# Optimization experiments

Hardware: AMD Instinct MI355X
Metric: run time of the kernel (lower is better)

## Reference

```python
import jax, jax.numpy as jnp
import numpy as np

SEQ_LEN = 8192
D_MODEL = 1024
D_K = 128
D_V = 128


def setup_inputs() -> dict:
    key = jax.random.key(0)
    kx, kq, kk, kv = jax.random.split(key, 4)
    # xavier-uniform scale for (out, in) linear weights
    def xavier(k, out_f, in_f):
        lim = np.sqrt(6.0 / (in_f + out_f))
        return jax.random.uniform(k, (out_f, in_f), jnp.float32, -lim, lim)
    return {
        "X": jax.random.normal(kx, (SEQ_LEN, D_MODEL), jnp.float32),
        "Wq": xavier(kq, D_K, D_MODEL),
        "Wk": xavier(kk, D_K, D_MODEL),
        "Wv": xavier(kv, D_V, D_MODEL),
    }


def reference(X, Wq, Wk, Wv):
    # X: (S, d_model); W*: (d_k, d_model) torch Linear weights (y = x @ W.T)
    S = X.shape[0]
    Q = X @ Wq.T                      # (S, d_k)
    K = X @ Wk.T                      # (S, d_k)
    V = X @ Wv.T                      # (S, d_v)
    scale = jnp.sqrt(jnp.asarray(D_K, X.dtype))
    scores = (Q @ K.T) / scale        # (S, S)
    causal = jnp.tril(jnp.ones((S, S), bool))
    scores = jnp.where(causal, scores, -jnp.inf)
    weights = jax.nn.softmax(scores, axis=1)
    # dropout p=0.0 -> identity
    Z = weights @ V                   # (S, d_v)
    return Z
```

## Files before the change

kernel.cpp:

```cpp
#include <hip/hip_runtime.h>
#include <hip/hip_bf16.h>

#define S_LEN 8192
#define DM    1024
#define DK    128
#define KSTR  136
#define VSTR  72
#define PSTR2 72
#define SLOTD 1056

typedef __attribute__((ext_vector_type(8))) short bf16x8;
typedef __attribute__((ext_vector_type(8))) _Float16 f16x8;
typedef __attribute__((ext_vector_type(4))) float f32x4;

__device__ __forceinline__ f32x4 mfma16(bf16x8 a, bf16x8 b, f32x4 c) {
    return __builtin_amdgcn_mfma_f32_16x16x32_bf16(a, b, c, 0, 0, 0);
}

__device__ __forceinline__ ushort f2bf(float f) {
    unsigned u = __builtin_bit_cast(unsigned, f);
    u += 0x7FFFu + ((u >> 16) & 1u);
    return (ushort)(u >> 16);
}

__device__ __forceinline__ ushort f2h(float f) {
    return __builtin_bit_cast(ushort, (_Float16)f);
}

__global__ __launch_bounds__(256, 1)
void convert_kernel(const float* __restrict__ X,
                    const float* __restrict__ Wq,
                    const float* __restrict__ Wk,
                    const float* __restrict__ Wv,
                    _Float16* __restrict__ Xh,
                    _Float16* __restrict__ Wh) {
    const int NX4 = S_LEN * DM / 4;
    const int NW4 = DK * DM / 4;
    const int total4 = NX4 + 3 * NW4;
    for (int i = blockIdx.x * 256 + threadIdx.x; i < total4; i += gridDim.x * 256) {
        const float4* src;
        _Float16* dst;
        int off;
        if (i < NX4) {
            src = (const float4*)X; dst = Xh; off = i;
        } else {
            const int w = i - NX4;
            const int which = w / NW4;
            off = w - which * NW4;
            src = (const float4*)(which == 0 ? Wq : (which == 1 ? Wk : Wv));
            dst = Wh + which * (DK * DM);
        }
        const float4 v = src[off];
        union { _Float16 h[4]; uint2 u; } p;
        p.h[0] = (_Float16)v.x; p.h[1] = (_Float16)v.y;
        p.h[2] = (_Float16)v.z; p.h[3] = (_Float16)v.w;
        *(uint2*)(dst + (size_t)off * 4) = p.u;
    }
}

__global__ __launch_bounds__(256)
void proj_gemm_kernel(const _Float16* __restrict__ Xh,
                      const _Float16* __restrict__ Wh,
                      ushort* __restrict__ Qb,
                      ushort* __restrict__ Kb,
                      ushort* __restrict__ Vtb) {
    __shared__ _Float16 Ash[32 * 32];
    __shared__ _Float16 Bsh[128 * 32];

    const int tid  = threadIdx.x;
    const int lane = tid & 63;
    const int quad = lane >> 4;
    const int l15  = lane & 15;
    const int wv   = tid >> 6;
    const int wm   = wv & 1;
    const int wn   = wv >> 1;
    const int m0   = blockIdx.x * 32;
    const int nb   = blockIdx.y;
    const _Float16* Wbase = Wh + nb * (DK * DM);

    f32x4 acc[4];
#pragma unroll
    for (int ni = 0; ni < 4; ++ni) acc[ni] = (f32x4){0.f, 0.f, 0.f, 0.f};

    for (int kk = 0; kk < DM; kk += 32) {
        __syncthreads();
        for (int s = tid; s < 640; s += 256) {
            if (s < 128) {
                const int row = s >> 2, sg = s & 3;
                __builtin_amdgcn_global_load_lds(
                    (const __attribute__((address_space(1))) void*)(Xh + (size_t)(m0 + row) * DM + kk + sg * 8),
                    (__attribute__((address_space(3))) void*)(Ash + s * 8), 16, 0, 0);
            } else {
                const int t = s - 128;
                const int row = t >> 2, sg = t & 3;
                __builtin_amdgcn_global_load_lds(
                    (const __attribute__((address_space(1))) void*)(Wbase + (size_t)row * DM + kk + sg * 8),
                    (__attribute__((address_space(3))) void*)(Bsh + t * 8), 16, 0, 0);
            }
        }
        __syncthreads();

        const f16x8 af = *(const f16x8*)(Ash + (wm * 16 + l15) * 32 + quad * 8);
        f16x8 bf[4];
#pragma unroll
        for (int t = 0; t < 4; ++t)
            bf[t] = *(const f16x8*)(Bsh + (wn * 64 + t * 16 + l15) * 32 + quad * 8);
#pragma unroll
        for (int ni = 0; ni < 4; ++ni)
            acc[ni] = __builtin_amdgcn_mfma_f32_16x16x32_f16(af, bf[ni], acc[ni], 0, 0, 0);
    }

    if (nb == 2) {
#pragma unroll
        for (int ni = 0; ni < 4; ++ni) {
            const int n = wn * 64 + ni * 16 + l15;
            const int m = m0 + wm * 16 + quad * 4;
            union { ushort h[4]; uint2 u; } p;
#pragma unroll
            for (int r = 0; r < 4; ++r) p.h[r] = f2bf(acc[ni][r]);
            *(uint2*)(Vtb + (size_t)n * S_LEN + m) = p.u;
        }
    } else {
        ushort* Ob = (nb == 0) ? Qb : Kb;
        const float sc = (nb == 0) ? 0.088388347648318447f * 1.4426950408889634f : 1.0f;
#pragma unroll
        for (int ni = 0; ni < 4; ++ni) {
            const int n = wn * 64 + ni * 16 + l15;
#pragma unroll
            for (int r = 0; r < 4; ++r) {
                const int m = m0 + wm * 16 + quad * 4 + r;
                Ob[(size_t)m * DK + n] = f2bf(acc[ni][r] * sc);
            }
        }
    }
}

__global__ __launch_bounds__(256, 3)
void flash_partial_kernel(const ushort* __restrict__ Qg,
                          const ushort* __restrict__ Kg,
                          const ushort* __restrict__ Vtg,
                          float* __restrict__ Part) {
    __shared__ __align__(16) ushort Ks [64 * KSTR];
    __shared__ __align__(16) ushort Vts[128 * VSTR];
    __shared__ __align__(16) ushort PlA[4 * 16 * PSTR2];

    const int b = 575 - (int)blockIdx.x;
    int g = 0;
    while (b >= 8 * (g + 1) * (g + 2)) ++g;
    const int idx   = b - 8 * g * (g + 1);
    const int qb    = 16 * g + idx / (g + 1);
    const int chunk = idx % (g + 1);
    const int nkt   = qb + 1;
    const int kt_lo = chunk * nkt / (g + 1);
    const int kt_hi = (chunk + 1) * nkt / (g + 1);

    const int tid  = threadIdx.x;
    const int wv   = tid >> 6;
    const int lane = tid & 63;
    const int quad = lane >> 4;
    const int l15  = lane & 15;
    const int q0w  = qb * 64 + wv * 16;
    ushort* Pl = PlA + wv * 16 * PSTR2;

    bf16x8 qf[4];
    {
        const ushort* qrow = Qg + (size_t)(q0w + l15) * DK + quad * 8;
#pragma unroll
        for (int kc = 0; kc < 4; ++kc) qf[kc] = *(const bf16x8*)(qrow + kc * 32);
    }

    const bf16x8 ones = {(short)0x3F80, (short)0x3F80, (short)0x3F80, (short)0x3F80,
                         (short)0x3F80, (short)0x3F80, (short)0x3F80, (short)0x3F80};

    float m_[4], l_[4];
#pragma unroll
    for (int r = 0; r < 4; ++r) { m_[r] = -__builtin_inff(); l_[r] = 0.f; }
    f32x4 acc[8];
#pragma unroll
    for (int d = 0; d < 8; ++d) acc[d] = (f32x4){0.f, 0.f, 0.f, 0.f};

    bf16x8 stg[8];
#define LOAD_TILE(K0)                                                          \
    {                                                                          \
        const int k0_ = (K0);                                                  \
        _Pragma("unroll")                                                      \
        for (int i = 0; i < 8; ++i) {                                          \
            const int c = tid + (i << 8);                                      \
            if (c < 1024) {                                                    \
                const int row = c >> 4, ch = c & 15;                           \
                stg[i] = *(const bf16x8*)(Kg + (size_t)(k0_ + row) * DK + ch * 8); \
            } else {                                                           \
                const int cc = c - 1024;                                       \
                const int row = cc >> 3, ch = cc & 7;                          \
                stg[i] = *(const bf16x8*)(Vtg + (size_t)row * S_LEN + k0_ + ch * 8); \
            }                                                                  \
        }                                                                      \
    }

    LOAD_TILE(kt_lo * 64)

    for (int kt = kt_lo; kt < kt_hi; ++kt) {
        const int k0 = kt * 64;

        __syncthreads();
#pragma unroll
        for (int i = 0; i < 8; ++i) {
            const int c = tid + (i << 8);
            if (c < 1024) {
                const int row = c >> 4, ch = c & 15;
                *(bf16x8*)(Ks + row * KSTR + ch * 8) = stg[i];
            } else {
                const int cc = c - 1024;
                const int row = cc >> 3, ch = cc & 7;
                *(bf16x8*)(Vts + row * VSTR + ch * 8) = stg[i];
            }
        }
        if (kt + 1 < kt_hi) LOAD_TILE((kt + 1) * 64)
        __syncthreads();

        f32x4 Sr[4];
#pragma unroll
        for (int nb = 0; nb < 4; ++nb) {
            Sr[nb] = (f32x4){0.f, 0.f, 0.f, 0.f};
            const ushort* kb = Ks + (nb * 16 + l15) * KSTR + quad * 8;
#pragma unroll
            for (int kc = 0; kc < 4; ++kc)
                Sr[nb] = mfma16(qf[kc], *(const bf16x8*)(kb + kc * 32), Sr[nb]);
        }

        if (k0 + 63 > q0w) {
#pragma unroll
            for (int nb = 0; nb < 4; ++nb) {
                const int kg = k0 + nb * 16 + l15;
#pragma unroll
                for (int r = 0; r < 4; ++r)
                    if (kg > q0w + quad * 4 + r) Sr[nb][r] = -__builtin_inff();
            }
        }

        float al[4];
#pragma unroll
        for (int r = 0; r < 4; ++r) {
            float v = m_[r];
#pragma unroll
            for (int nb = 0; nb < 4; ++nb) v = fmaxf(v, Sr[nb][r]);
            v = fmaxf(v, __shfl_xor(v, 1));
            v = fmaxf(v, __shfl_xor(v, 2));
            v = fmaxf(v, __shfl_xor(v, 4));
            v = fmaxf(v, __shfl_xor(v, 8));
            al[r] = exp2f(m_[r] - v);
            m_[r] = v;
        }
#pragma unroll
        for (int nb = 0; nb < 4; ++nb) {
#pragma unroll
            for (int r = 0; r < 4; ++r) {
                const float p = exp2f(Sr[nb][r] - m_[r]);
                Pl[(quad * 4 + r) * PSTR2 + nb * 16 + l15] = f2bf(p);
            }
        }
#pragma unroll
        for (int d = 0; d < 8; ++d)
#pragma unroll
            for (int r = 0; r < 4; ++r) acc[d][r] *= al[r];

        f32x4 sacc = (f32x4){0.f, 0.f, 0.f, 0.f};
#pragma unroll
        for (int kcp = 0; kcp < 2; ++kcp) {
            const bf16x8 pf = *(const bf16x8*)(Pl + l15 * PSTR2 + kcp * 32 + quad * 8);
            sacc = mfma16(pf, ones, sacc);
#pragma unroll
            for (int db = 0; db < 8; ++db) {
                const bf16x8 vf = *(const bf16x8*)(Vts + (db * 16 + l15) * VSTR + kcp * 32 + quad * 8);
                acc[db] = mfma16(pf, vf, acc[db]);
            }
        }
#pragma unroll
        for (int r = 0; r < 4; ++r) l_[r] = l_[r] * al[r] + sacc[r];
    }
#undef LOAD_TILE

    const int qt16 = qb * 4 + wv;
    float* slot = Part + (size_t)(qt16 * 8 + chunk) * SLOTD;
    if (l15 == 0) {
#pragma unroll
        for (int r = 0; r < 4; ++r) {
            slot[quad * 4 + r]      = m_[r];
            slot[16 + quad * 4 + r] = l_[r];
        }
    }
    uint* slotO = (uint*)(slot + 32);
#pragma unroll
    for (int d = 0; d < 8; ++d)
#pragma unroll
        for (int r = 0; r < 4; ++r) {
            const float v  = acc[d][r];
            const float vp = __shfl_xor(v, 1);
            if ((l15 & 1) == 0) {
                const int row = quad * 4 + r;
                const uint u = (uint)f2h(v) | ((uint)f2h(vp) << 16);
                slotO[(row * 128 + d * 16 + l15) >> 1] = u;
            }
        }
}

__global__ __launch_bounds__(256)
void flash_merge_kernel(const float* __restrict__ Part, float* __restrict__ Out) {
    __shared__ float Ms[16], Ls[16];
    __shared__ float Sc[8][16];
    const int qt = blockIdx.x;
    const int q0 = qt * 16;
    const int P  = (qt >> 6) + 1;
    const int tid = threadIdx.x;
    const float* base = Part + (size_t)qt * 8 * SLOTD;

    if (tid < 16) {
        float M = -__builtin_inff();
        for (int p = 0; p < P; ++p) M = fmaxf(M, base[p * SLOTD + tid]);
        float L = 0.f;
        for (int p = 0; p < P; ++p)
            L += base[p * SLOTD + 16 + tid] * exp2f(base[p * SLOTD + tid] - M);
        Ms[tid] = M; Ls[tid] = L;
    }
    __syncthreads();
    if (tid < 128) {
        const int p = tid >> 4, row = tid & 15;
        Sc[p][row] = (p < P) ? exp2f(base[p * SLOTD + row] - Ms[row]) : 0.f;
    }
    __syncthreads();

#pragma unroll
    for (int j = tid; j < 1024; j += 256) {
        const int row = j >> 6, c2 = j & 63;
        float o0 = 0.f, o1 = 0.f;
        for (int p = 0; p < P; ++p) {
            const uint u = ((const uint*)(base + p * SLOTD + 32))[row * 64 + c2];
            const float sc = Sc[p][row];
            o0 += (float)__builtin_bit_cast(_Float16, (ushort)(u & 0xFFFF)) * sc;
            o1 += (float)__builtin_bit_cast(_Float16, (ushort)(u >> 16)) * sc;
        }
        const float inv = 1.0f / Ls[row];
        float2 o; o.x = o0 * inv; o.y = o1 * inv;
        *(float2*)(Out + (size_t)(q0 + row) * DK + c2 * 2) = o;
    }
}

extern "C" void kernel_launch(void* const* d_in, const int* in_sizes, int n_in,
                              void* d_out, int out_size, void* d_ws, size_t ws_size,
                              hipStream_t stream) {
    const float* X  = (const float*)d_in[0];
    const float* Wq = (const float*)d_in[1];
    const float* Wk = (const float*)d_in[2];
    const float* Wv = (const float*)d_in[3];
    ushort* ws  = (ushort*)d_ws;
    ushort* Qb  = ws;
    ushort* Kb  = ws + (size_t)S_LEN * DK;
    ushort* Vtb = ws + 2 * (size_t)S_LEN * DK;
    _Float16* Xh = (_Float16*)(ws + 3 * (size_t)S_LEN * DK);
    _Float16* Wh = Xh + (size_t)S_LEN * DM;
    float* Part = (float*)Xh;
    float* Out = (float*)d_out;

    convert_kernel<<<1024, 256, 0, stream>>>(X, Wq, Wk, Wv, Xh, Wh);
    proj_gemm_kernel<<<dim3(256, 3), 256, 0, stream>>>(Xh, Wh, Qb, Kb, Vtb);
    flash_partial_kernel<<<576, 256, 0, stream>>>(Qb, Kb, Vtb, Part);
    flash_merge_kernel<<<512, 256, 0, stream>>>(Part, Out);
}
```

Measured before the change: 179.6 us.

## Process 32 query rows per wave to reuse K/V tiles across two blocks

Each wave now handles two 16-row query tiles (128 queries per block instead of 64), so every K fragment and V fragment read from LDS feeds two MFMAs. Grid halves to 288 blocks with a new triangular split schedule, waves skip fully masked key tiles, and LDS row strides are changed to reduce padding. This raises register pressure (launch bounds drop to 2 blocks per CU) and halves the block count, which may hurt occupancy and load balance.

```diff
diff --git a/kernel.cpp b/kernel.cpp
--- a/kernel.cpp
+++ b/kernel.cpp
@@ -4,9 +4,9 @@
 #define S_LEN 8192
 #define DM    1024
 #define DK    128
-#define KSTR  136
-#define VSTR  72
-#define PSTR2 72
+#define KSTR  132
+#define VSTR  68
+#define PSTR3 68
 #define SLOTD 1056
 
 typedef __attribute__((ext_vector_type(8))) short bf16x8;
@@ -135,49 +135,59 @@
     }
 }
 
-__global__ __launch_bounds__(256, 3)
+__global__ __launch_bounds__(256, 2)
 void flash_partial_kernel(const ushort* __restrict__ Qg,
                           const ushort* __restrict__ Kg,
                           const ushort* __restrict__ Vtg,
                           float* __restrict__ Part) {
     __shared__ __align__(16) ushort Ks [64 * KSTR];
     __shared__ __align__(16) ushort Vts[128 * VSTR];
-    __shared__ __align__(16) ushort PlA[4 * 16 * PSTR2];
-
-    const int b = 575 - (int)blockIdx.x;
-    int g = 0;
-    while (b >= 8 * (g + 1) * (g + 2)) ++g;
-    const int idx   = b - 8 * g * (g + 1);
-    const int qb    = 16 * g + idx / (g + 1);
-    const int chunk = idx % (g + 1);
-    const int nkt   = qb + 1;
-    const int kt_lo = chunk * nkt / (g + 1);
-    const int kt_hi = (chunk + 1) * nkt / (g + 1);
+    __shared__ __align__(16) ushort PlA[4 * 32 * PSTR3];
+
+    const int b = 287 - (int)blockIdx.x;
+    int h = 0;
+    while (b >= 4 * (h + 1) * (h + 2)) ++h;
+    const int idx   = b - 4 * h * (h + 1);
+    const int qb    = 8 * h + idx / (h + 1);
+    const int chunk = idx % (h + 1);
+    const int nkt   = 2 * (qb + 1);
+    const int kt_lo = chunk * nkt / (h + 1);
+    const int kt_hi = (chunk + 1) * nkt / (h + 1);
 
     const int tid  = threadIdx.x;
     const int wv   = tid >> 6;
     const int lane = tid & 63;
     const int quad = lane >> 4;
     const int l15  = lane & 15;
-    const int q0w  = qb * 64 + wv * 16;
-    ushort* Pl = PlA + wv * 16 * PSTR2;
-
-    bf16x8 qf[4];
+    const int q0w  = qb * 128 + wv * 32;
+    ushort* Pl = PlA + wv * 32 * PSTR3;
+
+    bf16x8 qfA[4], qfB[4];
     {
-        const ushort* qrow = Qg + (size_t)(q0w + l15) * DK + quad * 8;
-#pragma unroll
-        for (int kc = 0; kc < 4; ++kc) qf[kc] = *(const bf16x8*)(qrow + kc * 32);
+        const ushort* qa = Qg + (size_t)(q0w + l15) * DK + quad * 8;
+        const ushort* qb_ = Qg + (size_t)(q0w + 16 + l15) * DK + quad * 8;
+#pragma unroll
+        for (int kc = 0; kc < 4; ++kc) {
+            qfA[kc] = *(const bf16x8*)(qa + kc * 32);
+            qfB[kc] = *(const bf16x8*)(qb_ + kc * 32);
+        }
     }
 
     const bf16x8 ones = {(short)0x3F80, (short)0x3F80, (short)0x3F80, (short)0x3F80,
                          (short)0x3F80, (short)0x3F80, (short)0x3F80, (short)0x3F80};
 
-    float m_[4], l_[4];
-#pragma unroll
-    for (int r = 0; r < 4; ++r) { m_[r] = -__builtin_inff(); l_[r] = 0.f; }
-    f32x4 acc[8];
-#pragma unroll
-    for (int d = 0; d < 8; ++d) acc[d] = (f32x4){0.f, 0.f, 0.f, 0.f};
+    float mA[4], lA[4], mB[4], lB[4];
+#pragma unroll
+    for (int r = 0; r < 4; ++r) {
+        mA[r] = -__builtin_inff(); lA[r] = 0.f;
+        mB[r] = -__builtin_inff(); lB[r] = 0.f;
+    }
+    f32x4 accA[8], accB[8];
+#pragma unroll
+    for (int d = 0; d < 8; ++d) {
+        accA[d] = (f32x4){0.f, 0.f, 0.f, 0.f};
+        accB[d] = (f32x4){0.f, 0.f, 0.f, 0.f};
+    }
 
     bf16x8 stg[8];
 #define LOAD_TILE(K0)                                                          \
@@ -218,14 +228,20 @@
         if (kt + 1 < kt_hi) LOAD_TILE((kt + 1) * 64)
         __syncthreads();
 
-        f32x4 Sr[4];
+        if (k0 > q0w + 31) continue;
+
+        f32x4 SA[4], SB[4];
 #pragma unroll
         for (int nb = 0; nb < 4; ++nb) {
-            Sr[nb] = (f32x4){0.f, 0.f, 0.f, 0.f};
+            SA[nb] = (f32x4){0.f, 0.f, 0.f, 0.f};
+            SB[nb] = (f32x4){0.f, 0.f, 0.f, 0.f};
             const ushort* kb = Ks + (nb * 16 + l15) * KSTR + quad * 8;
 #pragma unroll
-            for (int kc = 0; kc < 4; ++kc)
-                Sr[nb] = mfma16(qf[kc], *(const bf16x8*)(kb + kc * 32), Sr[nb]);
+            for (int kc = 0; kc < 4; ++kc) {
+                const bf16x8 kf = *(const bf16x8*)(kb + kc * 32);
+                SA[nb] = mfma16(qfA[kc], kf, SA[nb]);
+                SB[nb] = mfma16(qfB[kc], kf, SB[nb]);
+            }
         }
 
         if (k0 + 63 > q0w) {
@@ -234,74 +250,108 @@
                 const int kg = k0 + nb * 16 + l15;
 #pragma unroll
                 for (int r = 0; r < 4; ++r)
-                    if (kg > q0w + quad * 4 + r) Sr[nb][r] = -__builtin_inff();
-            }
-        }
-
-        float al[4];
+                    if (kg > q0w + quad * 4 + r) SA[nb][r] = -__builtin_inff();
+            }
+        }
+        if (k0 + 63 > q0w + 16) {
+#pragma unroll
+            for (int nb = 0; nb < 4; ++nb) {
+                const int kg = k0 + nb * 16 + l15;
+#pragma unroll
+                for (int r = 0; r < 4; ++r)
+                    if (kg > q0w + 16 + quad * 4 + r) SB[nb][r] = -__builtin_inff();
+            }
+        }
+
+        float alA[4], alB[4];
 #pragma unroll
         for (int r = 0; r < 4; ++r) {
-            float v = m_[r];
-#pragma unroll
-            for (int nb = 0; nb < 4; ++nb) v = fmaxf(v, Sr[nb][r]);
+            float v = mA[r];
+#pragma unroll
+            for (int nb = 0; nb < 4; ++nb) v = fmaxf(v, SA[nb][r]);
             v = fmaxf(v, __shfl_xor(v, 1));
             v = fmaxf(v, __shfl_xor(v, 2));
             v = fmaxf(v, __shfl_xor(v, 4));
             v = fmaxf(v, __shfl_xor(v, 8));
-            al[r] = exp2f(m_[r] - v);
-            m_[r] = v;
+            alA[r] = exp2f(mA[r] - v);
+            mA[r] = v;
+            float w = mB[r];
+#pragma unroll
+            for (int nb = 0; nb < 4; ++nb) w = fmaxf(w, SB[nb][r]);
+            w = fmaxf(w, __shfl_xor(w, 1));
+            w = fmaxf(w, __shfl_xor(w, 2));
+            w = fmaxf(w, __shfl_xor(w, 4));
+            w = fmaxf(w, __shfl_xor(w, 8));
+            alB[r] = exp2f(mB[r] - w);
+            mB[r] = w;
         }
 #pragma unroll
         for (int nb = 0; nb < 4; ++nb) {
 #pragma unroll
             for (int r = 0; r < 4; ++r) {
-                const float p = exp2f(Sr[nb][r] - m_[r]);
-                Pl[(quad * 4 + r) * PSTR2 + nb * 16 + l15] = f2bf(p);
+                Pl[(quad * 4 + r) * PSTR3 + nb * 16 + l15]        = f2bf(exp2f(SA[nb][r] - mA[r]));
+                Pl[(16 + quad * 4 + r) * PSTR3 + nb * 16 + l15]   = f2bf(exp2f(SB[nb][r] - mB[r]));
             }
         }
 #pragma unroll
         for (int d = 0; d < 8; ++d)
 #pragma unroll
-            for (int r = 0; r < 4; ++r) acc[d][r] *= al[r];
-
-        f32x4 sacc = (f32x4){0.f, 0.f, 0.f, 0.f};
+            for (int r = 0; r < 4; ++r) {
+                accA[d][r] *= alA[r];
+                accB[d][r] *= alB[r];
+            }
+
+        f32x4 sA = (f32x4){0.f, 0.f, 0.f, 0.f};
+        f32x4 sB = (f32x4){0.f, 0.f, 0.f, 0.f};
 #pragma unroll
         for (int kcp = 0; kcp < 2; ++kcp) {
-            const bf16x8 pf = *(const bf16x8*)(Pl + l15 * PSTR2 + kcp * 32 + quad * 8);
-            sacc = mfma16(pf, ones, sacc);
+            const bf16x8 pA = *(const bf16x8*)(Pl + l15 * PSTR3 + kcp * 32 + quad * 8);
+            const bf16x8 pB = *(const bf16x8*)(Pl + (16 + l15) * PSTR3 + kcp * 32 + quad * 8);
+            sA = mfma16(pA, ones, sA);
+            sB = mfma16(pB, ones, sB);
 #pragma unroll
             for (int db = 0; db < 8; ++db) {
                 const bf16x8 vf = *(const bf16x8*)(Vts + (db * 16 + l15) * VSTR + kcp * 32 + quad * 8);
-                acc[db] = mfma16(pf, vf, acc[db]);
-            }
-        }
-#pragma unroll
-        for (int r = 0; r < 4; ++r) l_[r] = l_[r] * al[r] + sacc[r];
+                accA[db] = mfma16(pA, vf, accA[db]);
+                accB[db] = mfma16(pB, vf, accB[db]);
+            }
+        }
+#pragma unroll
+        for (int r = 0; r < 4; ++r) {
+            lA[r] = lA[r] * alA[r] + sA[r];
+            lB[r] = lB[r] * alB[r] + sB[r];
+        }
     }
 #undef LOAD_TILE
 
-    const int qt16 = qb * 4 + wv;
-    float* slot = Part + (size_t)(qt16 * 8 + chunk) * SLOTD;
-    if (l15 == 0) {
-#pragma unroll
-        for (int r = 0; r < 4; ++r) {
-            slot[quad * 4 + r]      = m_[r];
-            slot[16 + quad * 4 + r] = l_[r];
-        }
-    }
-    uint* slotO = (uint*)(slot + 32);
-#pragma unroll
-    for (int d = 0; d < 8; ++d)
-#pragma unroll
-        for (int r = 0; r < 4; ++r) {
-            const float v  = acc[d][r];
-            const float vp = __shfl_xor(v, 1);
-            if ((l15 & 1) == 0) {
-                const int row = quad * 4 + r;
-                const uint u = (uint)f2h(v) | ((uint)f2h(vp) << 16);
-                slotO[(row * 128 + d * 16 + l15) >> 1] = u;
-            }
-        }
+#pragma unroll
+    for (int t = 0; t < 2; ++t) {
+        const float* m_ = t ? mB : mA;
+        const float* l_ = t ? lB : lA;
+        const f32x4* ac = t ? accB : accA;
+        const int qt = qb * 8 + wv * 2 + t;
+        float* slot = Part + (size_t)(qt * 8 + chunk) * SLOTD;
+        if (l15 == 0) {
+#pragma unroll
+            for (int r = 0; r < 4; ++r) {
+                slot[quad * 4 + r]      = m_[r];
+                slot[16 + quad * 4 + r] = l_[r];
+            }
+        }
+        uint* slotO = (uint*)(slot + 32);
+#pragma unroll
+        for (int d = 0; d < 8; ++d)
+#pragma unroll
+            for (int r = 0; r < 4; ++r) {
+                const float v  = ac[d][r];
+                const float vp = __shfl_xor(v, 1);
+                if ((l15 & 1) == 0) {
+                    const int row = quad * 4 + r;
+                    const uint u = (uint)f2h(v) | ((uint)f2h(vp) << 16);
+                    slotO[(row * 128 + d * 16 + l15) >> 1] = u;
+                }
+            }
+    }
 }
 
 __global__ __launch_bounds__(256)
@@ -363,6 +413,6 @@
 
     convert_kernel<<<1024, 256, 0, stream>>>(X, Wq, Wk, Wv, Xh, Wh);
     proj_gemm_kernel<<<dim3(256, 3), 256, 0, stream>>>(Xh, Wh, Qb, Kb, Vtb);
-    flash_partial_kernel<<<576, 256, 0, stream>>>(Qb, Kb, Vtb, Part);
+    flash_partial_kernel<<<288, 256, 0, stream>>>(Qb, Kb, Vtb, Part);
     flash_merge_kernel<<<512, 256, 0, stream>>>(Part, Out);
 }
```

Result: slower. 241.1 us (+34.2%).
